# Kernel optimization log

Measured on AMD Instinct MI355X. Metric: run time of the kernel, lower is better.

The kernel has to match this reference:

```python
import jax, jax.numpy as jnp
import numpy as np


def setup_inputs() -> dict:
    key = jax.random.key(0)
    k1, k2 = jax.random.split(key)
    B, L1, L2, D = 64, 1024, 1024, 768
    sent = jax.random.normal(k1, (B, L1, D), dtype=jnp.float32)
    e = jax.random.normal(k2, (B, L2, L1), dtype=jnp.float32)
    return {"sent": sent, "e": e}


def reference(sent, e):
    # Stable softmax over last axis (alignment weights over L1),
    # then weighted pooling of sent: equivalent to es @ sent.
    es = jax.nn.softmax(e, axis=-1)              # [B, L2, L1]
    out = jnp.einsum('bql,bld->bqd', es, sent)   # [B, L2, D]
    return out
```

## Files before the change

kernel.cpp:

```cpp
#include <hip/hip_runtime.h>
#include <hip/hip_bf16.h>


#define B_  64
#define L1_ 1024
#define L2_ 1024
#define D_  768

typedef __attribute__((ext_vector_type(8))) short short8;
typedef __attribute__((ext_vector_type(4))) float f32x4;
typedef __attribute__((ext_vector_type(8))) unsigned short ushort8;

static __device__ __forceinline__ unsigned short f2bf(float x) {
  union { float f; unsigned int u; } c; c.f = x;
  unsigned int r = c.u + 0x7FFF + ((c.u >> 16) & 1);
  return (unsigned short)(r >> 16);
}

__global__ __launch_bounds__(256) void transpose_cast_kernel(const float* __restrict__ sent,
                                                             unsigned short* __restrict__ sT) {
  __shared__ unsigned short tile[64][66];
  const int b  = blockIdx.z;
  const int l0 = blockIdx.y << 6;
  const int d0 = blockIdx.x << 6;
  const int t  = threadIdx.x;
  const float* sp = sent + ((size_t)b * L1_ + l0) * D_ + d0;
  const int c4 = (t & 15) << 2;
  const int r0 = t >> 4;
#pragma unroll
  for (int p = 0; p < 4; ++p) {
    const int r = r0 + (p << 4);
    float4 v = *reinterpret_cast<const float4*>(sp + (size_t)r * D_ + c4);
    tile[r][c4 + 0] = f2bf(v.x);
    tile[r][c4 + 1] = f2bf(v.y);
    tile[r][c4 + 2] = f2bf(v.z);
    tile[r][c4 + 3] = f2bf(v.w);
  }
  __syncthreads();
  unsigned short* op = sT + ((size_t)b * D_ + d0) * L1_ + l0;
  const int l8  = (t & 7) << 3;
  const int dd0 = t >> 3;
#pragma unroll
  for (int p = 0; p < 2; ++p) {
    const int d = dd0 + (p << 5);
    ushort8 w;
#pragma unroll
    for (int j = 0; j < 8; ++j) w[j] = tile[l8 + j][d];
    *reinterpret_cast<ushort8*>(op + (size_t)d * L1_ + l8) = w;
  }
}

#define BM 128
#define BN 256
#define BK 32
#define NT    (L1_ / BK)
#define NTILE (D_ / BN)
#define MTILE (L2_ / BM)
#define NWG   (NTILE * MTILE * B_)

#define SW(r) ((((r) >> 2) ^ (r)) & 3)

#define GLOAD(gp, lp) \
  __builtin_amdgcn_global_load_lds((const __attribute__((address_space(1))) char*)(gp), \
                                   (__attribute__((address_space(3))) char*)(lp), 16, 0, 0)

#define LOADA(T) do { const int _ta = (T) & (NT - 1);                                        \
    aregs[0] = *reinterpret_cast<const float4*>(Ae + (size_t)rA * L1_ + _ta * BK + cA);      \
    aregs[1] = *reinterpret_cast<const float4*>(Ae + (size_t)rA * L1_ + _ta * BK + cA + 4);  \
  } while (0)

#define EXPWRITE(T) do { if ((T) < NT) {                                        \
    unsigned short* Ad_ = &As[(T) & 1][0];                                      \
    float ex_[8];                                                               \
    ex_[0] = __expf(aregs[0].x); ex_[1] = __expf(aregs[0].y);                   \
    ex_[2] = __expf(aregs[0].z); ex_[3] = __expf(aregs[0].w);                   \
    ex_[4] = __expf(aregs[1].x); ex_[5] = __expf(aregs[1].y);                   \
    ex_[6] = __expf(aregs[1].z); ex_[7] = __expf(aregs[1].w);                   \
    psum += ((ex_[0] + ex_[1]) + (ex_[2] + ex_[3]))                             \
          + ((ex_[4] + ex_[5]) + (ex_[6] + ex_[7]));                            \
    ushort8 w0_;                                                                \
    _Pragma("unroll")                                                           \
    for (int q_ = 0; q_ < 8; ++q_) w0_[q_] = f2bf(ex_[q_]);                     \
    *reinterpret_cast<ushort8*>(&Ad_[rA * BK + aslot * 8]) = w0_;               \
  } } while (0)

#define SB(T) do { if ((T) < NT) {                                              \
    GLOAD(Bb + (size_t)rB0 * L1_ + (T) * BK + sB0, &Bs[(T) & 1][(w * 32) * BK]);      \
    GLOAD(Bb + (size_t)rB1 * L1_ + (T) * BK + sB1, &Bs[(T) & 1][(w * 32 + 16) * BK]); \
  } } while (0)

__global__ __launch_bounds__(512, 2) void gemm_kernel(const float* __restrict__ e,
                                                      const unsigned short* __restrict__ sT,
                                                      float* __restrict__ out) {
  __shared__ __align__(16) unsigned short As[2][BM * BK];
  __shared__ __align__(16) unsigned short Bs[2][BN * BK];
  __shared__ float sArr[BM];

  const int orig = blockIdx.x;
  const int wgid = (orig & 7) * (NWG / 8) + (orig >> 3);
  const int b    = wgid / (NTILE * MTILE);
  const int rem  = wgid % (NTILE * MTILE);
  const int m0   = (rem / NTILE) * BM;
  const int n0   = (rem % NTILE) * BN;

  const int t    = threadIdx.x;
  const int lane = t & 63;
  const int w    = t >> 6;
  const int wm   = w >> 2;
  const int wn   = w & 3;
  const int l15  = lane & 15;
  const int ksl  = lane >> 4;
  const int rA   = w * 16 + (lane >> 2);
  const int cA   = (lane & 3) * 8;
  const int aslot = (lane & 3) ^ SW(rA);
  const int rB0  = w * 32 + (lane >> 2);
  const int rB1  = rB0 + 16;
  const int sB0  = ((lane & 3) ^ SW(rB0)) * 8;
  const int sB1  = ((lane & 3) ^ SW(rB1)) * 8;

  const float*          Ae = e  + ((size_t)b * L2_ + m0) * L1_;
  const unsigned short* Bb = sT + ((size_t)b * D_  + n0) * L1_;

  f32x4 acc[4][4] = {};
  float4 aregs[2];
  float psum = 0.f;

  LOADA(0);
  SB(0);
  EXPWRITE(0);
  LOADA(1);
  asm volatile("s_waitcnt vmcnt(2) lgkmcnt(0)" ::: "memory");
  __builtin_amdgcn_s_barrier();
  __builtin_amdgcn_sched_barrier(0);

  for (int kt = 0; kt < NT; ++kt) {
    SB(kt + 1);
    EXPWRITE(kt + 1);
    LOADA(kt + 2);

    const unsigned short* Apt = As[kt & 1];
    const unsigned short* Bpt = Bs[kt & 1];
    short8 a[4], bb[4];
    __builtin_amdgcn_s_setprio(1);
#pragma unroll
    for (int i = 0; i < 4; ++i) {
      const int ra = wm * 64 + i * 16 + l15;
      a[i] = *reinterpret_cast<const short8*>(&Apt[ra * BK + ((ksl ^ SW(ra)) << 3)]);
      const int rb = wn * 64 + i * 16 + l15;
      bb[i] = *reinterpret_cast<const short8*>(&Bpt[rb * BK + ((ksl ^ SW(rb)) << 3)]);
    }
#pragma unroll
    for (int i = 0; i < 4; ++i)
#pragma unroll
      for (int jn = 0; jn < 4; ++jn)
        acc[i][jn] = __builtin_amdgcn_mfma_f32_16x16x32_bf16(a[i], bb[jn], acc[i][jn], 0, 0, 0);
    __builtin_amdgcn_s_setprio(0);

    if (kt < NT - 1) {
      asm volatile("s_waitcnt vmcnt(2) lgkmcnt(0)" ::: "memory");
      __builtin_amdgcn_s_barrier();
      __builtin_amdgcn_sched_barrier(0);
    }
  }

  psum += __shfl_xor(psum, 1);
  psum += __shfl_xor(psum, 2);
  if ((lane & 3) == 0) sArr[rA] = psum;
  __syncthreads();

  const int rbase = (lane >> 4) << 2;
  float* Cb = out + ((size_t)b * L2_ + m0 + wm * 64) * D_ + n0 + wn * 64;
#pragma unroll
  for (int i = 0; i < 4; ++i) {
    float inv[4];
#pragma unroll
    for (int r = 0; r < 4; ++r)
      inv[r] = 1.0f / sArr[wm * 64 + i * 16 + rbase + r];
#pragma unroll
    for (int jn = 0; jn < 4; ++jn)
#pragma unroll
      for (int r = 0; r < 4; ++r)
        Cb[(size_t)(i * 16 + rbase + r) * D_ + jn * 16 + l15] = acc[i][jn][r] * inv[r];
  }
}

extern "C" void kernel_launch(void* const* d_in, const int* in_sizes, int n_in,
                              void* d_out, int out_size, void* d_ws, size_t ws_size,
                              hipStream_t stream) {
  const float* sent = (const float*)d_in[0];
  const float* e    = (const float*)d_in[1];
  float* out = (float*)d_out;

  unsigned short* sT = (unsigned short*)d_ws;

  transpose_cast_kernel<<<dim3(D_ / 64, L1_ / 64, B_), 256, 0, stream>>>(sent, sT);
  gemm_kernel<<<dim3(NWG), 512, 0, stream>>>(e, sT, out);
}
```

Before: 261.1 us.

## Split exp into separate bf16 pass and use larger-tile bf16 GEMM

Measured after the change: 296.3 us. 1.13x slower.

```diff
diff --git a/kernel.cpp b/kernel.cpp
--- a/kernel.cpp
+++ b/kernel.cpp
@@ -10,12 +10,17 @@
 typedef __attribute__((ext_vector_type(8))) short short8;
 typedef __attribute__((ext_vector_type(4))) float f32x4;
 typedef __attribute__((ext_vector_type(8))) unsigned short ushort8;
+typedef __attribute__((ext_vector_type(4))) unsigned short ushort4v;
 
 static __device__ __forceinline__ unsigned short f2bf(float x) {
   union { float f; unsigned int u; } c; c.f = x;
   unsigned int r = c.u + 0x7FFF + ((c.u >> 16) & 1);
   return (unsigned short)(r >> 16);
 }
+
+#define GLOAD(gp, lp) \
+  __builtin_amdgcn_global_load_lds((const __attribute__((address_space(1))) char*)(gp), \
+                                   (__attribute__((address_space(3))) char*)(lp), 16, 0, 0)
 
 __global__ __launch_bounds__(256) void transpose_cast_kernel(const float* __restrict__ sent,
                                                              unsigned short* __restrict__ sT) {
@@ -50,6 +55,149 @@
   }
 }
 
+__global__ __launch_bounds__(256) void exp_rows_kernel(const float* __restrict__ e,
+                                                       unsigned short* __restrict__ expE,
+                                                       float* __restrict__ rsInv) {
+  const int t    = threadIdx.x;
+  const int lane = t & 63;
+  const int wv   = t >> 6;
+  const int rowb = blockIdx.x << 4;
+#pragma unroll
+  for (int i = 0; i < 4; ++i) {
+    const int row = rowb + (i << 2) + wv;
+    const float* rp = e + (size_t)row * L1_;
+    unsigned short* op = expE + (size_t)row * L1_;
+    float s = 0.f;
+#pragma unroll
+    for (int j = 0; j < 4; ++j) {
+      float4 v = *reinterpret_cast<const float4*>(rp + j * 256 + lane * 4);
+      float e0 = __expf(v.x), e1 = __expf(v.y), e2 = __expf(v.z), e3 = __expf(v.w);
+      s += (e0 + e1) + (e2 + e3);
+      ushort4v o;
+      o[0] = f2bf(e0); o[1] = f2bf(e1); o[2] = f2bf(e2); o[3] = f2bf(e3);
+      *reinterpret_cast<ushort4v*>(op + j * 256 + lane * 4) = o;
+    }
+#pragma unroll
+    for (int dd = 1; dd < 64; dd <<= 1) s += __shfl_xor(s, dd);
+    if (lane == 0) rsInv[row] = 1.0f / s;
+  }
+}
+
+#define BM2 256
+#define BN2 256
+#define BK2 64
+#define NT2   (L1_ / BK2)
+#define MT2   (L2_ / BM2)
+#define NTL2  (D_ / BN2)
+#define NWG2  (B_ * MT2 * NTL2)
+
+#define SA2(T, BUF) do { const int _tt = (T) & (NT2 - 1); \
+    _Pragma("unroll") \
+    for (int r_ = 0; r_ < 4; ++r_) \
+      GLOAD(Asrc2 + (size_t)r_ * 64 * L1_ + _tt * BK2, &As2[BUF][(r_ * 64 + w * 8) * BK2]); \
+  } while (0)
+#define SB2(T, BUF) do { const int _tt = (T) & (NT2 - 1); \
+    _Pragma("unroll") \
+    for (int r_ = 0; r_ < 4; ++r_) \
+      GLOAD(Bsrc2 + (size_t)r_ * 64 * L1_ + _tt * BK2, &Bs2[BUF][(r_ * 64 + w * 8) * BK2]); \
+  } while (0)
+
+#define PHASE2(RB, RH, KH, ...) do { \
+    __VA_ARGS__ \
+    short8 a_[4], b_[4]; \
+    _Pragma("unroll") \
+    for (int ii = 0; ii < 4; ++ii) { \
+      const int ra_ = wm * 128 + ((RH) * 4 + ii) * 16 + l15; \
+      a_[ii] = *reinterpret_cast<const short8*>( \
+          &As2[RB][ra_ * BK2 + ((((KH) * 4 + ksl) ^ (l15 & 7)) << 3)]); \
+      const int rb_ = wn * 64 + ii * 16 + l15; \
+      b_[ii] = *reinterpret_cast<const short8*>( \
+          &Bs2[RB][rb_ * BK2 + ((((KH) * 4 + ksl) ^ (l15 & 7)) << 3)]); \
+    } \
+    __builtin_amdgcn_sched_barrier(0); \
+    __builtin_amdgcn_s_barrier(); \
+    asm volatile("s_waitcnt lgkmcnt(0)" ::: "memory"); \
+    __builtin_amdgcn_sched_barrier(0); \
+    __builtin_amdgcn_s_setprio(1); \
+    _Pragma("unroll") \
+    for (int ii = 0; ii < 4; ++ii) \
+      _Pragma("unroll") \
+      for (int jj = 0; jj < 4; ++jj) \
+        acc[(RH) * 4 + ii][jj] = __builtin_amdgcn_mfma_f32_16x16x32_bf16( \
+            a_[ii], b_[jj], acc[(RH) * 4 + ii][jj], 0, 0, 0); \
+    __builtin_amdgcn_s_setprio(0); \
+    __builtin_amdgcn_sched_barrier(0); \
+    __builtin_amdgcn_s_barrier(); \
+  } while (0)
+
+#define TILE2(T, RB, SBUF) do { \
+    PHASE2(RB, 0, 0, SA2((T) + 1, SBUF); SB2((T) + 1, SBUF); ); \
+    PHASE2(RB, 0, 1, ; ); \
+    PHASE2(RB, 1, 0, ; ); \
+    PHASE2(RB, 1, 1, \
+        asm volatile("s_waitcnt vmcnt(0)" ::: "memory"); \
+        __builtin_amdgcn_sched_barrier(0); ); \
+  } while (0)
+
+__global__ __launch_bounds__(512, 2) void gemm2_kernel(const unsigned short* __restrict__ expE,
+                                                       const unsigned short* __restrict__ sT,
+                                                       const float* __restrict__ rsInv,
+                                                       float* __restrict__ out) {
+  __shared__ __align__(16) unsigned short As2[2][BM2 * BK2];
+  __shared__ __align__(16) unsigned short Bs2[2][BN2 * BK2];
+  __shared__ float sArr[BM2];
+
+  const int orig = blockIdx.x;
+  const int wgid = (orig & 7) * (NWG2 / 8) + (orig >> 3);
+  const int b    = wgid / (MT2 * NTL2);
+  const int rem  = wgid % (MT2 * NTL2);
+  const int m0   = (rem / NTL2) * BM2;
+  const int n0   = (rem % NTL2) * BN2;
+
+  const int t    = threadIdx.x;
+  const int lane = t & 63;
+  const int w    = t >> 6;
+  const int wm   = w >> 2;
+  const int wn   = w & 3;
+  const int l15  = lane & 15;
+  const int ksl  = lane >> 4;
+
+  const int srow  = w * 8 + (lane >> 3);
+  const int sslot = (lane & 7) ^ (lane >> 3);
+  const unsigned short* Asrc2 = expE + ((size_t)b * L2_ + m0 + srow) * L1_ + sslot * 8;
+  const unsigned short* Bsrc2 = sT   + ((size_t)b * D_  + n0 + srow) * L1_ + sslot * 8;
+
+  if (t < BM2) sArr[t] = rsInv[(size_t)b * L2_ + m0 + t];
+
+  f32x4 acc[8][4] = {};
+
+  SA2(0, 0); SB2(0, 0);
+  asm volatile("s_waitcnt vmcnt(0) lgkmcnt(0)" ::: "memory");
+  __builtin_amdgcn_s_barrier();
+  __builtin_amdgcn_sched_barrier(0);
+
+#pragma unroll 1
+  for (int kt = 0; kt < NT2; kt += 2) {
+    TILE2(kt,     0, 1);
+    TILE2(kt + 1, 1, 0);
+  }
+
+  const int rbase = (lane >> 4) << 2;
+  float* Cb = out + ((size_t)b * L2_ + m0 + wm * 128) * D_ + n0 + wn * 64;
+#pragma unroll
+  for (int i = 0; i < 8; ++i) {
+    float inv[4];
+#pragma unroll
+    for (int r = 0; r < 4; ++r)
+      inv[r] = sArr[wm * 128 + i * 16 + rbase + r];
+#pragma unroll
+    for (int jj = 0; jj < 4; ++jj)
+#pragma unroll
+      for (int r = 0; r < 4; ++r)
+        Cb[(size_t)(i * 16 + rbase + r) * D_ + jj * 16 + l15] = acc[i][jj][r] * inv[r];
+  }
+}
+
 #define BM 128
 #define BN 256
 #define BK 32
@@ -59,10 +207,6 @@
 #define NWG   (NTILE * MTILE * B_)
 
 #define SW(r) ((((r) >> 2) ^ (r)) & 3)
-
-#define GLOAD(gp, lp) \
-  __builtin_amdgcn_global_load_lds((const __attribute__((address_space(1))) char*)(gp), \
-                                   (__attribute__((address_space(3))) char*)(lp), 16, 0, 0)
 
 #define LOADA(T) do { const int _ta = (T) & (NT - 1);                                        \
     aregs[0] = *reinterpret_cast<const float4*>(Ae + (size_t)rA * L1_ + _ta * BK + cA);      \
@@ -89,9 +233,9 @@
     GLOAD(Bb + (size_t)rB1 * L1_ + (T) * BK + sB1, &Bs[(T) & 1][(w * 32 + 16) * BK]); \
   } } while (0)
 
-__global__ __launch_bounds__(512, 2) void gemm_kernel(const float* __restrict__ e,
-                                                      const unsigned short* __restrict__ sT,
-                                                      float* __restrict__ out) {
+__global__ __launch_bounds__(512, 2) void gemm_fused_kernel(const float* __restrict__ e,
+                                                            const unsigned short* __restrict__ sT,
+                                                            float* __restrict__ out) {
   __shared__ __align__(16) unsigned short As[2][BM * BK];
   __shared__ __align__(16) unsigned short Bs[2][BN * BK];
   __shared__ float sArr[BM];
@@ -191,8 +335,20 @@
   const float* e    = (const float*)d_in[1];
   float* out = (float*)d_out;
 
+  const size_t ST_BYTES   = (size_t)B_ * D_ * L1_ * 2;
+  const size_t EXPE_BYTES = (size_t)B_ * L2_ * L1_ * 2;
+  const size_t RS_BYTES   = (size_t)B_ * L2_ * 4;
+
   unsigned short* sT = (unsigned short*)d_ws;
 
   transpose_cast_kernel<<<dim3(D_ / 64, L1_ / 64, B_), 256, 0, stream>>>(sent, sT);
-  gemm_kernel<<<dim3(NWG), 512, 0, stream>>>(e, sT, out);
-}
+
+  if (ws_size >= ST_BYTES + EXPE_BYTES + RS_BYTES) {
+    unsigned short* expE  = (unsigned short*)((char*)d_ws + ST_BYTES);
+    float*          rsInv = (float*)((char*)d_ws + ST_BYTES + EXPE_BYTES);
+    exp_rows_kernel<<<dim3(B_ * L2_ / 16), 256, 0, stream>>>(e, expE, rsInv);
+    gemm2_kernel<<<dim3(NWG2), 512, 0, stream>>>(expE, sT, rsInv, out);
+  } else {
+    gemm_fused_kernel<<<dim3(NWG), 512, 0, stream>>>(e, sT, out);
+  }
+}
```
